# Kernel tuning notes

Hardware: AMD Instinct MI355X
Metric: run time of the kernel (lower is better)

The kernel has to match this reference:

```python
import jax, jax.numpy as jnp
import numpy as np

V, E, H, D_IMG, A = 32000, 512, 512, 2048, 128
PAD_ID = 0
LN_EPS = 1e-5


def setup_inputs() -> dict:
    key = jax.random.key(0)
    ks = jax.random.split(key, 20)
    B, S, T = 32, 49, 64
    s = 0.02
    embed = jax.random.normal(ks[0], (V, E), jnp.float32) * s
    embed = embed.at[PAD_ID].set(0.0)
    return {
        "img_seq": jax.random.normal(ks[1], (B, S, D_IMG), jnp.float32),
        "tokens_in": jax.random.randint(ks[2], (B, T), 0, V, jnp.int64),
        "embed": embed,
        "W_ctx": jax.random.normal(ks[3], (E, D_IMG), jnp.float32) * s,
        "W_mix": jax.random.normal(ks[4], (E, 2 * E), jnp.float32) * s,
        "ln_g": jnp.ones((E,), jnp.float32),
        "ln_b": jnp.zeros((E,), jnp.float32),
        "W_ih": jax.random.normal(ks[5], (4 * H, E), jnp.float32) * s,
        "W_hh": jax.random.normal(ks[6], (4 * H, H), jnp.float32) * s,
        "b_ih": jnp.zeros((4 * H,), jnp.float32),
        "b_hh": jnp.zeros((4 * H,), jnp.float32),
        "W_head": jax.random.normal(ks[7], (V, H), jnp.float32) * s,
        "W_img": jax.random.normal(ks[8], (A, D_IMG), jnp.float32) * s,
        "W_hid": jax.random.normal(ks[9], (A, H), jnp.float32) * s,
        "w_score": jax.random.normal(ks[10], (A,), jnp.float32) * s,
        "W_h0": jax.random.normal(ks[11], (H, D_IMG), jnp.float32) * s,
        "b_h0": jnp.zeros((H,), jnp.float32),
        "W_c0": jax.random.normal(ks[12], (H, D_IMG), jnp.float32) * s,
        "b_c0": jnp.zeros((H,), jnp.float32),
    }


def _decode(img_seq, tokens_in, embed, W_ctx, W_mix, ln_g, ln_b,
            W_ih, W_hh, b_ih, b_hh, W_head, W_img, W_hid, w_score,
            W_h0, b_h0, W_c0, b_c0):
    # precompute image projection: [B,S,A]
    proj_image = jnp.einsum('bsd,ad->bsa', img_seq, W_img)
    g = img_seq.mean(1)  # [B, D_img]
    h = jnp.tanh(g @ W_h0.T + b_h0) * 0.5
    c = jnp.tanh(g @ W_c0.T + b_c0) * 0.5

    def step(carry, tok_t):
        h, c = carry
        emb = embed[tok_t] * (tok_t != PAD_ID)[:, None].astype(embed.dtype)
        # additive attention
        ph = h @ W_hid.T  # [B,A]
        comb = jnp.tanh(proj_image + ph[:, None, :])  # [B,S,A]
        scores = jnp.einsum('bsa,a->bs', comb, w_score)
        w = jax.nn.softmax(scores, axis=-1)
        ctx = jnp.einsum('bs,bsd->bd', w, img_seq)
        ctxE = ctx @ W_ctx.T
        x = jnp.concatenate([emb, ctxE], axis=-1) @ W_mix.T
        x = jax.nn.relu(x)
        mu = x.mean(-1, keepdims=True)
        var = ((x - mu) ** 2).mean(-1, keepdims=True)
        x = (x - mu) * jax.lax.rsqrt(var + LN_EPS) * ln_g + ln_b
        x = x + emb
        # LSTMCell (torch gate order: i, f, g, o)
        gates = x @ W_ih.T + b_ih + h @ W_hh.T + b_hh
        i_, f_, g_, o_ = jnp.split(gates, 4, axis=-1)
        c2 = jax.nn.sigmoid(f_) * c + jax.nn.sigmoid(i_) * jnp.tanh(g_)
        h2 = jax.nn.sigmoid(o_) * jnp.tanh(c2)
        logits = h2 @ W_head.T
        return (h2, c2), logits

    _, outs = jax.lax.scan(step, (h, c), tokens_in.T)  # [T,B,V]
    return jnp.transpose(outs, (1, 0, 2))  # [B,T,V]


def reference(img_seq, tokens_in, embed, W_ctx, W_mix, ln_g, ln_b,
              W_ih, W_hh, b_ih, b_hh, W_head, W_img, W_hid, w_score,
              W_h0, b_h0, W_c0, b_c0):
    return _decode(img_seq, tokens_in, embed, W_ctx, W_mix, ln_g, ln_b,
                   W_ih, W_hh, b_ih, b_hh, W_head, W_img, W_hid, w_score,
                   W_h0, b_h0, W_c0, b_c0)
```

## Files before the change

### kernel.cpp

```cpp
#include <hip/hip_runtime.h>

#define NV 32000
#define NT 64
#define NBLK 256u

typedef unsigned long long ull;
typedef unsigned short ushort;
typedef __attribute__((ext_vector_type(8))) short v8s;
typedef __attribute__((ext_vector_type(4))) float v4f;

#define WS_WBF     0
#define WS_H2BF    8192000
#define WS_IMGEM   8716288
#define WS_PROJ    9568256
#define WS_EMBM    9781248
#define WS_WHHBF   10829824
#define WS_WIHBF   11354112
#define WS_WHIDBF  11878400
#define WS_H       11911168
#define WS_XN      11943936
#define WS_C       11960320
#define WS_FLAGS   11976704
#define WS_G       11979264
#define PS_IMGBF   0
#define PS_WCTXBF  1703936
#define PS_WIMGBF  2228224
#define PS_WMIXRBF 2359296
#define PS_WMIXLBF 2490368
#define PS_IMGEBF  3342336

__device__ __forceinline__ float fsig(float x) {
    x = fminf(fmaxf(x, -30.f), 30.f);
    return 1.f / (1.f + __expf(-x));
}
__device__ __forceinline__ float ftanh(float x) {
    x = fminf(fmaxf(x, -15.f), 15.f);
    float e = __expf(2.f * x);
    return (e - 1.f) / (e + 1.f);
}
__device__ __forceinline__ unsigned short f2bf(float f) {
    union { float f; unsigned int u; } v; v.f = f;
    unsigned int u = v.u;
    return (unsigned short)((u + 0x7FFFu + ((u >> 16) & 1u)) >> 16);
}
__device__ __forceinline__ unsigned pkf(float x, float y) {
    return (unsigned)f2bf(x) | ((unsigned)f2bf(y) << 16);
}
__device__ __forceinline__ float bf_lo(unsigned u) { return __uint_as_float(u << 16); }
__device__ __forceinline__ float bf_hi(unsigned u) { return __uint_as_float(u & 0xffff0000u); }
__device__ __forceinline__ ull agld(const ull* p) {
    return __hip_atomic_load(p, __ATOMIC_RELAXED, __HIP_MEMORY_SCOPE_AGENT);
}
__device__ __forceinline__ unsigned pk2(ull v) {
    return (unsigned)f2bf(__uint_as_float((unsigned)v)) |
           ((unsigned)f2bf(__uint_as_float((unsigned)(v >> 32))) << 16);
}


__global__ __launch_bounds__(256) void k_castall(
        const float* __restrict__ img, const float* __restrict__ Wctx,
        const float* __restrict__ Wimg, const float* __restrict__ Wmix,
        const float* __restrict__ Whh, const float* __restrict__ Wih,
        const float* __restrict__ Whid,
        ushort* __restrict__ imgbf, ushort* __restrict__ wctxbf,
        ushort* __restrict__ wimgbf, ushort* __restrict__ wmixRbf,
        ushort* __restrict__ wmixLbf, ushort* __restrict__ whhbf,
        ushort* __restrict__ wihbf, ushort* __restrict__ whidbf,
        unsigned* __restrict__ flg) {
    int blk = blockIdx.x, tid = threadIdx.x;
    if (blk >= 3616) {
        for (int i = tid; i < 2560; i += 256) flg[i] = 0u;
        return;
    }
    const float* in; ushort* out; int R, K, ldi, off;
    if (blk < 1664)      { in = img;  out = imgbf;   R = 1568; K = 2048; ldi = 2048; off = 0; }
    else if (blk < 2176) { in = Wctx; out = wctxbf;  R = 512;  K = 2048; ldi = 2048; off = 0;   blk -= 1664; }
    else if (blk < 2304) { in = Wimg; out = wimgbf;  R = 128;  K = 2048; ldi = 2048; off = 0;   blk -= 2176; }
    else if (blk < 2432) { in = Wmix; out = wmixRbf; R = 512;  K = 512;  ldi = 1024; off = 512; blk -= 2304; }
    else if (blk < 2560) { in = Wmix; out = wmixLbf; R = 512;  K = 512;  ldi = 1024; off = 0;   blk -= 2432; }
    else if (blk < 3072) { in = Whh;  out = whhbf;   R = 2048; K = 512;  ldi = 512;  off = 0;   blk -= 2560; }
    else if (blk < 3584) { in = Wih;  out = wihbf;   R = 2048; K = 512;  ldi = 512;  off = 0;   blk -= 3072; }
    else                 { in = Whid; out = whidbf;  R = 128;  K = 512;  ldi = 512;  off = 0;   blk -= 3584; }
    size_t i = ((size_t)blk * 256 + tid) * 8;
    int r = (int)(i / K), k = (int)(i % K);
    uint4 o = {0, 0, 0, 0};
    if (r < R) {
        const float* p = in + (size_t)r * ldi + off + k;
        float4 a = *(const float4*)(p);
        float4 b = *(const float4*)(p + 4);
        o.x = pkf(a.x, a.y); o.y = pkf(a.z, a.w);
        o.z = pkf(b.x, b.y); o.w = pkf(b.z, b.w);
    }
    *(uint4*)(out + i) = o;
}

__global__ __launch_bounds__(256) void k_gemm(const ushort* __restrict__ A,
        const ushort* __restrict__ B, float* __restrict__ C, int N, int K) {
    __shared__ ushort Al[128][72];
    __shared__ ushort Bl[128][72];
    int n0 = blockIdx.x * 128, m0 = blockIdx.y * 128;
    int tid = threadIdx.x, lane = tid & 63, wid = tid >> 6;
    int wm = wid >> 1, wn = wid & 1;
    v4f acc[4][4] = {};
    for (int kt = 0; kt < K; kt += 64) {
        __syncthreads();
        #pragma unroll
        for (int i = 0; i < 4; i++) {
            int idx = i * 256 + tid;
            int row = idx >> 3, c8 = (idx & 7) * 8;
            *(uint4*)&Al[row][c8] = *(const uint4*)&A[(size_t)(m0 + row) * K + kt + c8];
            *(uint4*)&Bl[row][c8] = *(const uint4*)&B[(size_t)(n0 + row) * K + kt + c8];
        }
        __syncthreads();
        #pragma unroll
        for (int kk = 0; kk < 2; kk++) {
            v8s a[4], bfr[4];
            int ko = kk * 32 + (lane >> 4) * 8;
            #pragma unroll
            for (int mi = 0; mi < 4; mi++)
                a[mi] = *(const v8s*)&Al[wm * 64 + mi * 16 + (lane & 15)][ko];
            #pragma unroll
            for (int ni = 0; ni < 4; ni++)
                bfr[ni] = *(const v8s*)&Bl[wn * 64 + ni * 16 + (lane & 15)][ko];
            #pragma unroll
            for (int mi = 0; mi < 4; mi++)
                #pragma unroll
                for (int ni = 0; ni < 4; ni++)
                    acc[mi][ni] = __builtin_amdgcn_mfma_f32_16x16x32_bf16(a[mi], bfr[ni], acc[mi][ni], 0, 0, 0);
        }
    }
    int col = lane & 15, rbase = (lane >> 4) * 4;
    #pragma unroll
    for (int mi = 0; mi < 4; mi++)
        #pragma unroll
        for (int ni = 0; ni < 4; ni++)
            #pragma unroll
            for (int r = 0; r < 4; r++) {
                int m = m0 + wm * 64 + mi * 16 + rbase + r;
                int v = n0 + wn * 64 + ni * 16 + col;
                C[(size_t)m * N + v] = acc[mi][ni][r];
            }
}

__global__ __launch_bounds__(256) void k_gemm3(
        const ushort* __restrict__ imgbf, const ushort* __restrict__ wctxbf,
        const ushort* __restrict__ wimgbf, const float* __restrict__ embed,
        const int* __restrict__ toks, const ushort* __restrict__ wmixLbf,
        ushort* __restrict__ imgEbf, float* __restrict__ proj,
        float* __restrict__ embM) {
    __shared__ ushort Al[128][72];
    __shared__ ushort Bl[128][72];
    int bid = blockIdx.x;
    const ushort* A; const ushort* B; int mode, K, N, n0, m0;
    if (bid < 52)      { mode = 0; A = imgbf; B = wctxbf;  K = 2048; N = 512; n0 = (bid & 3) * 128; m0 = (bid >> 2) * 128; }
    else if (bid < 65) { mode = 1; A = imgbf; B = wimgbf;  K = 2048; N = 128; n0 = 0;               m0 = (bid - 52) * 128; }
    else { int e = bid - 65; mode = 2; A = nullptr; B = wmixLbf; K = 512; N = 512; n0 = (e & 3) * 128; m0 = (e >> 2) * 128; }
    int tid = threadIdx.x, lane = tid & 63, wid = tid >> 6;
    int wm = wid >> 1, wn = wid & 1;
    v4f acc[4][4] = {};
    for (int kt = 0; kt < K; kt += 64) {
        __syncthreads();
        #pragma unroll
        for (int i = 0; i < 4; i++) {
            int idx = i * 256 + tid;
            int row = idx >> 3, c8 = (idx & 7) * 8;
            if (mode == 2) {
                int rowg = m0 + row;
                int tok = toks[(rowg & 31) * 64 + (rowg >> 5)];
                uint4 oa = {0, 0, 0, 0};
                if (tok != 0) {
                    const float* pa = embed + (size_t)tok * 512 + kt + c8;
                    float4 a0 = *(const float4*)pa, a1 = *(const float4*)(pa + 4);
                    oa.x = pkf(a0.x, a0.y); oa.y = pkf(a0.z, a0.w);
                    oa.z = pkf(a1.x, a1.y); oa.w = pkf(a1.z, a1.w);
                }
                *(uint4*)&Al[row][c8] = oa;
            } else {
                *(uint4*)&Al[row][c8] = *(const uint4*)&A[(size_t)(m0 + row) * K + kt + c8];
            }
            *(uint4*)&Bl[row][c8] = *(const uint4*)&B[(size_t)(n0 + row) * K + kt + c8];
        }
        __syncthreads();
        #pragma unroll
        for (int kk = 0; kk < 2; kk++) {
            v8s a[4], bfr[4];
            int ko = kk * 32 + (lane >> 4) * 8;
            #pragma unroll
            for (int mi = 0; mi < 4; mi++)
                a[mi] = *(const v8s*)&Al[wm * 64 + mi * 16 + (lane & 15)][ko];
            #pragma unroll
            for (int ni = 0; ni < 4; ni++)
                bfr[ni] = *(const v8s*)&Bl[wn * 64 + ni * 16 + (lane & 15)][ko];
            #pragma unroll
            for (int mi = 0; mi < 4; mi++)
                #pragma unroll
                for (int ni = 0; ni < 4; ni++)
                    acc[mi][ni] = __builtin_amdgcn_mfma_f32_16x16x32_bf16(a[mi], bfr[ni], acc[mi][ni], 0, 0, 0);
        }
    }
    int col = lane & 15, rbase = (lane >> 4) * 4;
    #pragma unroll
    for (int mi = 0; mi < 4; mi++)
        #pragma unroll
        for (int ni = 0; ni < 4; ni++)
            #pragma unroll
            for (int r = 0; r < 4; r++) {
                int m = m0 + wm * 64 + mi * 16 + rbase + r;
                int v = n0 + wn * 64 + ni * 16 + col;
                if (mode == 0)      imgEbf[(size_t)m * 512 + v] = f2bf(acc[mi][ni][r]);
                else if (mode == 1) proj[(size_t)m * 128 + v] = acc[mi][ni][r];
                else                embM[(size_t)m * 512 + v] = acc[mi][ni][r];
            }
}

__global__ __launch_bounds__(256) void k_gmean(const float* __restrict__ img,
                                               float* __restrict__ g) {
    int b = blockIdx.x;
    for (int d = threadIdx.x; d < 2048; d += 256) {
        float s = 0.f;
        for (int ss = 0; ss < 49; ss++) s += img[((size_t)(b * 49 + ss)) * 2048 + d];
        g[b * 2048 + d] = s * (1.f / 49.f);
    }
}

__global__ __launch_bounds__(256) void k_h0c0(const float* __restrict__ g,
        const float* __restrict__ Wh0, const float* __restrict__ bh0,
        const float* __restrict__ Wc0, const float* __restrict__ bc0,
        float* __restrict__ h0, float* __restrict__ c0) {
    int b = blockIdx.x >> 2, m = (blockIdx.x >> 1) & 1, rh = blockIdx.x & 1;
    __shared__ float gs[2048];
    for (int d = threadIdx.x; d < 2048; d += 256) gs[d] = g[b * 2048 + d];
    __syncthreads();
    const float* W = m ? Wc0 : Wh0;
    const float* bb = m ? bc0 : bh0;
    float* out = m ? c0 : h0;
    int r = rh * 256 + threadIdx.x;
    float acc = 0.f;
    const float* wr = W + (size_t)r * 2048;
    for (int d = 0; d < 2048; d += 4) {
        float4 w = *(const float4*)(wr + d);
        acc += w.x * gs[d] + w.y * gs[d + 1] + w.z * gs[d + 2] + w.w * gs[d + 3];
    }
    out[b * 512 + r] = ftanh(acc + bb[r]) * 0.5f;
}


__device__ __forceinline__ void waitflags(unsigned* FLG, int base, int stride,
                                          int n, unsigned tgt) {
    if (threadIdx.x < 64) {
        bool done;
        do {
            unsigned v = tgt;
            if ((int)threadIdx.x < n)
                v = __hip_atomic_load(FLG + (base + (int)threadIdx.x * stride) * 16,
                                      __ATOMIC_RELAXED, __HIP_MEMORY_SCOPE_AGENT);
            done = __all((int)(v >= tgt));
            if (!done) __builtin_amdgcn_s_sleep(1);
        } while (!done);
    }
    __syncthreads();
}

template <int SLP>
__device__ __forceinline__ void waitgates(unsigned* FLG, unsigned tgt) {
    if (threadIdx.x < 64) {
        bool done;
        do {
            unsigned v0 = __hip_atomic_load(FLG + threadIdx.x * 16,
                            __ATOMIC_RELAXED, __HIP_MEMORY_SCOPE_AGENT);
            unsigned v1 = __hip_atomic_load(FLG + (threadIdx.x + 64) * 16,
                            __ATOMIC_RELAXED, __HIP_MEMORY_SCOPE_AGENT);
            done = __all((int)(v0 >= tgt && v1 >= tgt));
            if (!done) __builtin_amdgcn_s_sleep(SLP);
        } while (!done);
    }
    __syncthreads();
}

__device__ __forceinline__ void waitcast(unsigned* FLG) {
    if (threadIdx.x == 0) {
        while (__hip_atomic_load(FLG + 12, __ATOMIC_RELAXED, __HIP_MEMORY_SCOPE_AGENT) < 96u)
            __builtin_amdgcn_s_sleep(4);
    }
    __syncthreads();
}

union SMem {
    struct {
        ushort wh[64][520];
        ushort wi[64][520];
        ushort hsb[16][520];
        float gtmp[4][16][16];
        ushort h2s[16][8];
    } g;
    struct {
        float imgem[49][512];
        float projl[49][128];
        float hb[512];
        float ebs[512];
        float php[8][128];
        float ph[128];
        float scp[64][16];
        float wsm[64];
        float xps[2][512];
        float wred[8][2];
        float bc[2];
    } a;
    struct {
        ushort Al[256][72];
        ushort Bl[128][72];
    } h;
};

__device__ __forceinline__ void head_tile(SMem& sm, const ushort* __restrict__ h2bf,
        const ushort* __restrict__ Wbf, float* __restrict__ out, int m0, int n0) {
    int tid = threadIdx.x, lane = tid & 63, wid = tid >> 6;
    int wm = wid >> 1, wn = wid & 1;
    v4f acc[4][4] = {};
    for (int kt = 0; kt < 512; kt += 64) {
        __syncthreads();
        #pragma unroll
        for (int i = 0; i < 2; i++) {
            int idx = i * 1024 + tid;
            int row = idx >> 3, c8 = (idx & 7) * 8;
            const ull* p = (const ull*)&h2bf[(size_t)(m0 + row) * 512 + kt + c8];
            ull v0 = agld(p), v1 = agld(p + 1);
            *(ull*)&sm.h.Al[row][c8] = v0;
            *(ull*)&sm.h.Al[row][c8 + 4] = v1;
        }
        {
            int row = tid >> 3, c8 = (tid & 7) * 8;
            *(uint4*)&sm.h.Bl[row][c8] = *(const uint4*)&Wbf[(size_t)(n0 + row) * 512 + kt + c8];
        }
        __syncthreads();
        if (wid < 8) {
            #pragma unroll
            for (int kk = 0; kk < 2; kk++) {
                v8s a[4], bfr[4];
                int ko = kk * 32 + (lane >> 4) * 8;
                #pragma unroll
                for (int mi = 0; mi < 4; mi++)
                    a[mi] = *(const v8s*)&sm.h.Al[wm * 64 + mi * 16 + (lane & 15)][ko];
                #pragma unroll
                for (int ni = 0; ni < 4; ni++)
                    bfr[ni] = *(const v8s*)&sm.h.Bl[wn * 64 + ni * 16 + (lane & 15)][ko];
                #pragma unroll
                for (int mi = 0; mi < 4; mi++)
                    #pragma unroll
                    for (int ni = 0; ni < 4; ni++)
                        acc[mi][ni] = __builtin_amdgcn_mfma_f32_16x16x32_bf16(a[mi], bfr[ni], acc[mi][ni], 0, 0, 0);
            }
        }
    }
    if (wid < 8) {
        int col = lane & 15, rbase = (lane >> 4) * 4;
        #pragma unroll
        for (int mi = 0; mi < 4; mi++)
            #pragma unroll
            for (int ni = 0; ni < 4; ni++)
                #pragma unroll
                for (int r = 0; r < 4; r++) {
                    int m = m0 + wm * 64 + mi * 16 + rbase + r;
                    int v = n0 + wn * 64 + ni * 16 + col;
                    int b = m & 31, t = m >> 5;
                    out[((size_t)(b * 64 + t)) * 32000 + v] = acc[mi][ni][r];
                }
    }
}

__global__ __launch_bounds__(1024, 1) void k_persist(
        const int* __restrict__ toks, const float* __restrict__ embed,
        const float* __restrict__ lng, const float* __restrict__ lnb,
        const float* __restrict__ bih, const float* __restrict__ bhh,
        const float* __restrict__ wsc, const ushort* __restrict__ whidbf,
        const ushort* __restrict__ whhbf, const ushort* __restrict__ wihbf,
        const float* __restrict__ proj, const float* __restrict__ imgEM,
        const float* __restrict__ embM, float* __restrict__ H,
        const float* __restrict__ C0, float* __restrict__ XN,
        unsigned* __restrict__ FLG, ushort* __restrict__ h2bf,
        const float* __restrict__ W_head, ushort* __restrict__ Wbf,
        float* __restrict__ out) {
    __shared__ SMem sm;
    __shared__ unsigned sh_w;
    int blk = blockIdx.x, tid = threadIdx.x;

    if (blk < 128) {
        int jc = blk >> 2, bg = blk & 3, b0 = bg * 8;
        int wid = tid >> 6, lane = tid & 63;
        int gate = wid & 3;
        for (int i = tid; i < 4096; i += 1024) {
            int rr = i >> 6, c8 = (i & 63) * 8;
            size_t R = (size_t)((rr >> 4) * 512 + jc * 16 + (rr & 15)) * 512 + c8;
            *(uint4*)&sm.g.wh[rr][c8] = *(const uint4*)&whhbf[R];
            *(uint4*)&sm.g.wi[rr][c8] = *(const uint4*)&wihbf[R];
        }
        for (int i = tid; i < 2080; i += 1024) ((ull*)sm.g.hsb)[i] = 0;
        float c_reg = 0.f, bs0 = 0.f, bs1 = 0.f, bs2 = 0.f, bs3 = 0.f;
        if (tid < 128) {
            int jl = tid >> 3, bb = tid & 7;
            int j = jc * 16 + jl;
            c_reg = C0[(b0 + bb) * 512 + j];
            bs0 = bih[j] + bhh[j];
            bs1 = bih[512 + j] + bhh[512 + j];
            bs2 = bih[1024 + j] + bhh[1024 + j];
            bs3 = bih[1536 + j] + bhh[1536 + j];
        }
        __syncthreads();

        for (int t = 0; t < NT; t++) {
            waitflags(FLG, bg, 4, 32, (unsigned)t);
            {
                const float* Hb = H + (t & 1) * 16384 + b0 * 512;
                if (tid < 512) {
                    int bb = tid >> 6, c8 = (tid & 63) * 8;
                    const ull* p = (const ull*)(Hb + bb * 512 + c8);
                    uint4 o = { pk2(agld(p)), pk2(agld(p + 1)),
                                pk2(agld(p + 2)), pk2(agld(p + 3)) };
                    *(uint4*)&sm.g.hsb[bb][c8] = o;
                }
            }
            __syncthreads();
            v4f acc = {};
            if (wid < 4) {
                #pragma unroll
                for (int ks = 0; ks < 16; ks++) {
                    int ko = ks * 32 + (lane >> 4) * 8;
                    v8s a = *(const v8s*)&sm.g.hsb[lane & 15][ko];
                    v8s b = *(const v8s*)&sm.g.wh[gate * 16 + (lane & 15)][ko];
                    acc = __builtin_amdgcn_mfma_f32_16x16x32_bf16(a, b, acc, 0, 0, 0);
                }
            }
            waitflags(FLG, 128 + b0, 1, 8, (unsigned)(t + 1));
            {
                const float* Xb = XN + b0 * 512;
                if (tid < 512) {
                    int bb = tid >> 6, c8 = (tid & 63) * 8;
                    const ull* p = (const ull*)(Xb + bb * 512 + c8);
                    uint4 o = { pk2(agld(p)), pk2(agld(p + 1)),
                                pk2(agld(p + 2)), pk2(agld(p + 3)) };
                    *(uint4*)&sm.g.hsb[bb][c8] = o;
                }
            }
            __syncthreads();
            if (wid < 4) {
                #pragma unroll
                for (int ks = 0; ks < 16; ks++) {
                    int ko = ks * 32 + (lane >> 4) * 8;
                    v8s a = *(const v8s*)&sm.g.hsb[lane & 15][ko];
                    v8s b = *(const v8s*)&sm.g.wi[gate * 16 + (lane & 15)][ko];
                    acc = __builtin_amdgcn_mfma_f32_16x16x32_bf16(a, b, acc, 0, 0, 0);
                }
                #pragma unroll
                for (int q = 0; q < 4; q++)
                    sm.g.gtmp[gate][lane & 15][(lane >> 4) * 4 + q] = acc[q];
            }
            __syncthreads();
            if (tid < 128) {
                int jl = tid >> 3, bb = tid & 7;
                float vi = sm.g.gtmp[0][jl][bb] + bs0;
                float vf = sm.g.gtmp[1][jl][bb] + bs1;
                float vg = sm.g.gtmp[2][jl][bb] + bs2;
                float vo = sm.g.gtmp[3][jl][bb] + bs3;
                float c2 = fsig(vf) * c_reg + fsig(vi) * ftanh(vg);
                float h2 = fsig(vo) * ftanh(c2);
                c_reg = c2;
                int bglob = b0 + bb, j = jc * 16 + jl;
                __hip_atomic_store((unsigned*)&H[((t + 1) & 1) * 16384 + bglob * 512 + j],
                                   __float_as_uint(h2), __ATOMIC_RELAXED, __HIP_MEMORY_SCOPE_AGENT);
                sm.g.h2s[jl][bb] = f2bf(h2);
            }
            __syncthreads();
            if (tid < 64) {
                int jlp = tid >> 3, bb = tid & 7;
                unsigned pk = (unsigned)sm.g.h2s[2 * jlp][bb]
                            | ((unsigned)sm.g.h2s[2 * jlp + 1][bb] << 16);
                int bglob = b0 + bb, j = jc * 16 + 2 * jlp;
                __hip_atomic_store((unsigned*)&h2bf[(size_t)(t * 32 + bglob) * 512 + j],
                                   pk, __ATOMIC_RELAXED, __HIP_MEMORY_SCOPE_AGENT);
            }
            __syncthreads();
            if (tid == 0)
                __hip_atomic_store(FLG + blk * 16, (unsigned)(t + 1),
                                   __ATOMIC_RELAXED, __HIP_MEMORY_SCOPE_AGENT);
        }
    } else if (blk < 160) {
        int b = blk - 128, bgb = b >> 3;
        for (int i = tid; i < 49 * 512; i += 1024)
            sm.a.imgem[i >> 9][i & 511] = imgEM[(size_t)b * 49 * 512 + i];
        for (int i = tid; i < 49 * 128; i += 1024)
            sm.a.projl[i >> 7][i & 127] = proj[(size_t)b * 49 * 128 + i];
        __syncthreads();
        for (int t = 0; t < NT; t++) {
            waitflags(FLG, bgb, 4, 32, (unsigned)t);
            int tok = toks[b * 64 + t];
            if (tid < 256) {
                ull v = agld((const ull*)(H + (t & 1) * 16384) + b * 256 + tid);
                *(ull*)&sm.a.hb[tid * 2] = v;
            } else if (tid < 768) {
                int k = tid - 256;
                sm.a.ebs[k] = (tok == 0) ? 0.f : embed[(size_t)tok * 512 + k];
            }
            __syncthreads();
            {
                int a = tid & 127, kq = tid >> 7;
                const ushort* wr2 = whidbf + (size_t)a * 512 + kq * 64;
                const float* hp = sm.a.hb + kq * 64;
                float p = 0.f;
                #pragma unroll
                for (int k = 0; k < 64; k += 8) {
                    uint4 q = *(const uint4*)(wr2 + k);
                    float4 ha = *(const float4*)(hp + k);
                    float4 hb4 = *(const float4*)(hp + k + 4);
                    p += bf_lo(q.x)*ha.x + bf_hi(q.x)*ha.y + bf_lo(q.y)*ha.z + bf_hi(q.y)*ha.w
                       + bf_lo(q.z)*hb4.x + bf_hi(q.z)*hb4.y + bf_lo(q.w)*hb4.z + bf_hi(q.w)*hb4.w;
                }
                sm.a.php[kq][a] = p;
            }
            __syncthreads();
            if (tid < 128) {
                float p = 0.f;
                #pragma unroll
                for (int kq = 0; kq < 8; kq++) p += sm.a.php[kq][tid];
                sm.a.ph[tid] = p;
            }
            __syncthreads();
            {
                int s = tid >> 4, aq = tid & 15;
                float p = 0.f;
                if (s < 49) {
                    const float* pr = &sm.a.projl[s][aq * 8];
                    #pragma unroll
                    for (int a = 0; a < 8; a++)
                        p += ftanh(pr[a] + sm.a.ph[aq * 8 + a]) * wsc[aq * 8 + a];
                }
                sm.a.scp[s][aq] = p;
            }
            __syncthreads();
            if (tid < 64) {
                float v = 0.f;
                #pragma unroll
                for (int q = 0; q < 16; q++) v += sm.a.scp[tid][q];
                if (tid >= 49) v = -1e30f;
                float m = v;
                for (int o = 32; o > 0; o >>= 1) m = fmaxf(m, __shfl_xor(m, o));
                float e = (tid < 49) ? __expf(v - m) : 0.f;
                float su = e;
                for (int o = 32; o > 0; o >>= 1) su += __shfl_xor(su, o);
                sm.a.wsm[tid] = e / su;
            }
            __syncthreads();
            {
                int e = tid & 511, sh = tid >> 9;
                float xp = 0.f;
                if (sh == 0) xp = embM[(size_t)(t * 32 + b) * 512 + e];
                int s0 = sh * 25, s1 = sh ? 49 : 25;
                for (int s = s0; s < s1; s++)
                    xp += sm.a.wsm[s] * sm.a.imgem[s][e];
                sm.a.xps[sh][e] = xp;
            }
            __syncthreads();
            if (tid < 512) {
                float x = fmaxf(sm.a.xps[0][tid] + sm.a.xps[1][tid], 0.f);
                float s = x, s2 = x * x;
                for (int o = 32; o > 0; o >>= 1) { s += __shfl_xor(s, o); s2 += __shfl_xor(s2, o); }
                if ((tid & 63) == 0) { sm.a.wred[tid >> 6][0] = s; sm.a.wred[tid >> 6][1] = s2; }
            }
            __syncthreads();
            if (tid == 0) {
                float s = 0.f, s2 = 0.f;
                #pragma unroll
                for (int w = 0; w < 8; w++) { s += sm.a.wred[w][0]; s2 += sm.a.wred[w][1]; }
                float mu = s * (1.f / 512.f);
                float var = s2 * (1.f / 512.f) - mu * mu;
                sm.a.bc[0] = mu; sm.a.bc[1] = rsqrtf(var + 1e-5f);
            }
            __syncthreads();
            if (tid < 512) {
                float x = fmaxf(sm.a.xps[0][tid] + sm.a.xps[1][tid], 0.f);
                float xn = (x - sm.a.bc[0]) * sm.a.bc[1] * lng[tid] + lnb[tid] + sm.a.ebs[tid];
                __hip_atomic_store((unsigned*)&XN[b * 512 + tid], __float_as_uint(xn),
                                   __ATOMIC_RELAXED, __HIP_MEMORY_SCOPE_AGENT);
            }
            __syncthreads();
            if (tid == 0)
                __hip_atomic_store(FLG + (128 + b) * 16, (unsigned)(t + 1),
                                   __ATOMIC_RELAXED, __HIP_MEMORY_SCOPE_AGENT);
        }
    } else {
        int hb = blk - 160;
        {
            ull* wq = (ull*)Wbf;
            for (size_t i = (size_t)hb * 1024 + tid; i < 4096000; i += 98304) {
                const float* p = W_head + i * 4;
                float4 a = *(const float4*)p;
                ull v = (ull)pkf(a.x, a.y) | ((ull)pkf(a.z, a.w) << 32);
                __hip_atomic_store(wq + i, v, __ATOMIC_RELAXED, __HIP_MEMORY_SCOPE_AGENT);
            }
            __syncthreads();
            if (tid == 0)
                __hip_atomic_fetch_add(FLG + 12, 1u, __ATOMIC_RELAXED,
                                       __HIP_MEMORY_SCOPE_AGENT);
        }
        waitcast(FLG);
        unsigned have = 0;
        for (int w = hb; w < 1750; w += 96) {
            int mt = w / 250, nt = w % 250;
            unsigned need = (unsigned)(mt * 8 + 8);
            if (have < need) { waitgates<8>(FLG, need); have = need; }
            head_tile(sm, h2bf, (const ushort*)Wbf, out, mt * 256, nt * 128);
        }
    }

    waitgates<2>(FLG, (unsigned)NT);
    waitcast(FLG);
    for (;;) {
        if (tid == 0)
            sh_w = __hip_atomic_fetch_add(FLG + 8, 1u, __ATOMIC_RELAXED,
                                          __HIP_MEMORY_SCOPE_AGENT);
        __syncthreads();
        unsigned w = sh_w;
        __syncthreads();
        if (w >= 250u) break;
        head_tile(sm, h2bf, (const ushort*)Wbf, out, 7 * 256, (int)w * 128);
    }
}

extern "C" void kernel_launch(void* const* d_in, const int* in_sizes, int n_in,
                              void* d_out, int out_size, void* d_ws, size_t ws_size,
                              hipStream_t stream) {
    const float* img    = (const float*)d_in[0];
    const int*   toks   = (const int*)d_in[1];
    const float* embed  = (const float*)d_in[2];
    const float* W_ctx  = (const float*)d_in[3];
    const float* W_mix  = (const float*)d_in[4];
    const float* ln_g   = (const float*)d_in[5];
    const float* ln_b   = (const float*)d_in[6];
    const float* W_ih   = (const float*)d_in[7];
    const float* W_hh   = (const float*)d_in[8];
    const float* b_ih   = (const float*)d_in[9];
    const float* b_hh   = (const float*)d_in[10];
    const float* W_head = (const float*)d_in[11];
    const float* W_img  = (const float*)d_in[12];
    const float* W_hid  = (const float*)d_in[13];
    const float* w_sc   = (const float*)d_in[14];
    const float* W_h0   = (const float*)d_in[15];
    const float* b_h0   = (const float*)d_in[16];
    const float* W_c0   = (const float*)d_in[17];
    const float* b_c0   = (const float*)d_in[18];

    float* out = (float*)d_out;
    float* ws  = (float*)d_ws;
    ushort* Wbf    = (ushort*)(ws + WS_WBF);
    ushort* h2bf   = (ushort*)(ws + WS_H2BF);
    float*  imgEM  = ws + WS_IMGEM;
    float*  proj   = ws + WS_PROJ;
    float*  embM   = ws + WS_EMBM;
    ushort* whhbf  = (ushort*)(ws + WS_WHHBF);
    ushort* wihbf  = (ushort*)(ws + WS_WIHBF);
    ushort* whidbf = (ushort*)(ws + WS_WHIDBF);
    float*  H      = ws + WS_H;
    float*  XN     = ws + WS_XN;
    float*  C      = ws + WS_C;
    unsigned* flg  = (unsigned*)(ws + WS_FLAGS);
    float*  g      = ws + WS_G;
    ushort* imgbf   = (ushort*)(ws + PS_IMGBF);
    ushort* wctxbf  = (ushort*)(ws + PS_WCTXBF);
    ushort* wimgbf  = (ushort*)(ws + PS_WIMGBF);
    ushort* wmixRbf = (ushort*)(ws + PS_WMIXRBF);
    ushort* wmixLbf = (ushort*)(ws + PS_WMIXLBF);
    ushort* imgEbf  = (ushort*)(ws + PS_IMGEBF);

    k_castall<<<3617, 256, 0, stream>>>(img, W_ctx, W_img, W_mix, W_hh, W_ih, W_hid,
                                        imgbf, wctxbf, wimgbf, wmixRbf, wmixLbf,
                                        whhbf, wihbf, whidbf, flg);
    k_gemm3<<<129, 256, 0, stream>>>(imgbf, wctxbf, wimgbf, embed, toks, wmixLbf,
                                     imgEbf, proj, embM);
    k_gemm<<<dim3(4, 13), 256, 0, stream>>>(imgEbf, wmixRbf, imgEM, 512, 512);
    k_gmean<<<32, 256, 0, stream>>>(img, g);
    k_h0c0<<<128, 256, 0, stream>>>(g, W_h0, b_h0, W_c0, b_c0, H, C);

    k_persist<<<NBLK, 1024, 0, stream>>>(toks, embed, ln_g, ln_b, b_ih, b_hh, w_sc,
                                         whidbf, whhbf, wihbf, proj, imgEM, embM,
                                         H, C, XN, flg, h2bf, W_head, Wbf, out);
}
```

Before: 906.7 us.

## Fold h0/c0 init into batched MFMA gemm and store LN output as bf16

Removes the separate scalar fp32 h0/c0 kernel. W_h0 and W_c0 are now cast to bf16 in the cast kernel, and the h0/c0 projections run as extra MFMA tile blocks inside k_gemm3, with tanh applied in the epilogue. Separately, the layer-normed x vector exchanged between blocks each step is now written as packed bf16 instead of fp32, which halves the cross-block traffic on the recurrent critical path. The costs are extra cast work, padded 128-row tiles for only 32 real rows, and bf16 rounding of h0/c0.

```diff
diff --git a/kernel.cpp b/kernel.cpp
--- a/kernel.cpp
+++ b/kernel.cpp
@@ -28,6 +28,8 @@
 #define PS_WMIXRBF 2359296
 #define PS_WMIXLBF 2490368
 #define PS_IMGEBF  3342336
+#define PS_WH0BF   3768320
+#define PS_WC0BF   4292608
 
 __device__ __forceinline__ float fsig(float x) {
     x = fminf(fmaxf(x, -30.f), 30.f);
@@ -61,14 +63,16 @@
         const float* __restrict__ img, const float* __restrict__ Wctx,
         const float* __restrict__ Wimg, const float* __restrict__ Wmix,
         const float* __restrict__ Whh, const float* __restrict__ Wih,
-        const float* __restrict__ Whid,
+        const float* __restrict__ Whid, const float* __restrict__ Wh0,
+        const float* __restrict__ Wc0,
         ushort* __restrict__ imgbf, ushort* __restrict__ wctxbf,
         ushort* __restrict__ wimgbf, ushort* __restrict__ wmixRbf,
         ushort* __restrict__ wmixLbf, ushort* __restrict__ whhbf,
         ushort* __restrict__ wihbf, ushort* __restrict__ whidbf,
+        ushort* __restrict__ wh0bf, ushort* __restrict__ wc0bf,
         unsigned* __restrict__ flg) {
     int blk = blockIdx.x, tid = threadIdx.x;
-    if (blk >= 3616) {
+    if (blk >= 4640) {
         for (int i = tid; i < 2560; i += 256) flg[i] = 0u;
         return;
     }
@@ -80,7 +84,9 @@
     else if (blk < 2560) { in = Wmix; out = wmixLbf; R = 512;  K = 512;  ldi = 1024; off = 0;   blk -= 2432; }
     else if (blk < 3072) { in = Whh;  out = whhbf;   R = 2048; K = 512;  ldi = 512;  off = 0;   blk -= 2560; }
     else if (blk < 3584) { in = Wih;  out = wihbf;   R = 2048; K = 512;  ldi = 512;  off = 0;   blk -= 3072; }
-    else                 { in = Whid; out = whidbf;  R = 128;  K = 512;  ldi = 512;  off = 0;   blk -= 3584; }
+    else if (blk < 3616) { in = Whid; out = whidbf;  R = 128;  K = 512;  ldi = 512;  off = 0;   blk -= 3584; }
+    else if (blk < 4128) { in = Wh0;  out = wh0bf;   R = 512;  K = 2048; ldi = 2048; off = 0;   blk -= 3616; }
+    else                 { in = Wc0;  out = wc0bf;   R = 512;  K = 2048; ldi = 2048; off = 0;   blk -= 4128; }
     size_t i = ((size_t)blk * 256 + tid) * 8;
     int r = (int)(i / K), k = (int)(i % K);
     uint4 o = {0, 0, 0, 0};
@@ -146,15 +152,21 @@
         const ushort* __restrict__ imgbf, const ushort* __restrict__ wctxbf,
         const ushort* __restrict__ wimgbf, const float* __restrict__ embed,
         const int* __restrict__ toks, const ushort* __restrict__ wmixLbf,
+        const ushort* __restrict__ wh0bf, const ushort* __restrict__ wc0bf,
+        const float* __restrict__ g, const float* __restrict__ bh0,
+        const float* __restrict__ bc0,
         ushort* __restrict__ imgEbf, float* __restrict__ proj,
-        float* __restrict__ embM) {
+        float* __restrict__ embM, float* __restrict__ Hout,
+        float* __restrict__ Cout) {
     __shared__ ushort Al[128][72];
     __shared__ ushort Bl[128][72];
     int bid = blockIdx.x;
     const ushort* A; const ushort* B; int mode, K, N, n0, m0;
-    if (bid < 52)      { mode = 0; A = imgbf; B = wctxbf;  K = 2048; N = 512; n0 = (bid & 3) * 128; m0 = (bid >> 2) * 128; }
-    else if (bid < 65) { mode = 1; A = imgbf; B = wimgbf;  K = 2048; N = 128; n0 = 0;               m0 = (bid - 52) * 128; }
-    else { int e = bid - 65; mode = 2; A = nullptr; B = wmixLbf; K = 512; N = 512; n0 = (e & 3) * 128; m0 = (e >> 2) * 128; }
+    if (bid < 52)       { mode = 0; A = imgbf; B = wctxbf;  K = 2048; N = 512; n0 = (bid & 3) * 128; m0 = (bid >> 2) * 128; }
+    else if (bid < 65)  { mode = 1; A = imgbf; B = wimgbf;  K = 2048; N = 128; n0 = 0;               m0 = (bid - 52) * 128; }
+    else if (bid < 129) { int e = bid - 65;  mode = 2; A = nullptr; B = wmixLbf; K = 512;  N = 512; n0 = (e & 3) * 128; m0 = (e >> 2) * 128; }
+    else if (bid < 133) { mode = 3; A = nullptr; B = wh0bf; K = 2048; N = 512; n0 = (bid - 129) * 128; m0 = 0; }
+    else                { mode = 4; A = nullptr; B = wc0bf; K = 2048; N = 512; n0 = (bid - 133) * 128; m0 = 0; }
     int tid = threadIdx.x, lane = tid & 63, wid = tid >> 6;
     int wm = wid >> 1, wn = wid & 1;
     v4f acc[4][4] = {};
@@ -175,6 +187,16 @@
                     oa.z = pkf(a1.x, a1.y); oa.w = pkf(a1.z, a1.w);
                 }
                 *(uint4*)&Al[row][c8] = oa;
+            } else if (mode >= 3) {
+                int rowg = m0 + row;
+                uint4 oa = {0, 0, 0, 0};
+                if (rowg < 32) {
+                    const float* pa = g + (size_t)rowg * 2048 + kt + c8;
+                    float4 a0 = *(const float4*)pa, a1 = *(const float4*)(pa + 4);
+                    oa.x = pkf(a0.x, a0.y); oa.y = pkf(a0.z, a0.w);
+                    oa.z = pkf(a1.x, a1.y); oa.w = pkf(a1.z, a1.w);
+                }
+                *(uint4*)&Al[row][c8] = oa;
             } else {
                 *(uint4*)&Al[row][c8] = *(const uint4*)&A[(size_t)(m0 + row) * K + kt + c8];
             }
@@ -209,7 +231,13 @@
                 int v = n0 + wn * 64 + ni * 16 + col;
                 if (mode == 0)      imgEbf[(size_t)m * 512 + v] = f2bf(acc[mi][ni][r]);
                 else if (mode == 1) proj[(size_t)m * 128 + v] = acc[mi][ni][r];
-                else                embM[(size_t)m * 512 + v] = acc[mi][ni][r];
+                else if (mode == 2) embM[(size_t)m * 512 + v] = acc[mi][ni][r];
+                else if (m < 32) {
+                    float pre = acc[mi][ni][r] + ((mode == 3) ? bh0[v] : bc0[v]);
+                    float val = ftanh(pre) * 0.5f;
+                    if (mode == 3) Hout[m * 512 + v] = val;
+                    else           Cout[m * 512 + v] = val;
+                }
             }
 }
 
@@ -221,27 +249,6 @@
         for (int ss = 0; ss < 49; ss++) s += img[((size_t)(b * 49 + ss)) * 2048 + d];
         g[b * 2048 + d] = s * (1.f / 49.f);
     }
-}
-
-__global__ __launch_bounds__(256) void k_h0c0(const float* __restrict__ g,
-        const float* __restrict__ Wh0, const float* __restrict__ bh0,
-        const float* __restrict__ Wc0, const float* __restrict__ bc0,
-        float* __restrict__ h0, float* __restrict__ c0) {
-    int b = blockIdx.x >> 2, m = (blockIdx.x >> 1) & 1, rh = blockIdx.x & 1;
-    __shared__ float gs[2048];
-    for (int d = threadIdx.x; d < 2048; d += 256) gs[d] = g[b * 2048 + d];
-    __syncthreads();
-    const float* W = m ? Wc0 : Wh0;
-    const float* bb = m ? bc0 : bh0;
-    float* out = m ? c0 : h0;
-    int r = rh * 256 + threadIdx.x;
-    float acc = 0.f;
-    const float* wr = W + (size_t)r * 2048;
-    for (int d = 0; d < 2048; d += 4) {
-        float4 w = *(const float4*)(wr + d);
-        acc += w.x * gs[d] + w.y * gs[d + 1] + w.z * gs[d + 2] + w.w * gs[d + 3];
-    }
-    out[b * 512 + r] = ftanh(acc + bb[r]) * 0.5f;
 }
 
 
@@ -376,7 +383,7 @@
         const ushort* __restrict__ whhbf, const ushort* __restrict__ wihbf,
         const float* __restrict__ proj, const float* __restrict__ imgEM,
         const float* __restrict__ embM, float* __restrict__ H,
-        const float* __restrict__ C0, float* __restrict__ XN,
+        const float* __restrict__ C0, ushort* __restrict__ XNh,
         unsigned* __restrict__ FLG, ushort* __restrict__ h2bf,
         const float* __restrict__ W_head, ushort* __restrict__ Wbf,
         float* __restrict__ out) {
@@ -432,13 +439,13 @@
             }
             waitflags(FLG, 128 + b0, 1, 8, (unsigned)(t + 1));
             {
-                const float* Xb = XN + b0 * 512;
+                const ushort* Xh = XNh + b0 * 512;
                 if (tid < 512) {
                     int bb = tid >> 6, c8 = (tid & 63) * 8;
-                    const ull* p = (const ull*)(Xb + bb * 512 + c8);
-                    uint4 o = { pk2(agld(p)), pk2(agld(p + 1)),
-                                pk2(agld(p + 2)), pk2(agld(p + 3)) };
-                    *(uint4*)&sm.g.hsb[bb][c8] = o;
+                    const ull* p = (const ull*)(Xh + bb * 512 + c8);
+                    ull v0 = agld(p), v1 = agld(p + 1);
+                    *(ull*)&sm.g.hsb[bb][c8] = v0;
+                    *(ull*)&sm.g.hsb[bb][c8 + 4] = v1;
                 }
             }
             __syncthreads();
@@ -578,8 +585,12 @@
             if (tid < 512) {
                 float x = fmaxf(sm.a.xps[0][tid] + sm.a.xps[1][tid], 0.f);
                 float xn = (x - sm.a.bc[0]) * sm.a.bc[1] * lng[tid] + lnb[tid] + sm.a.ebs[tid];
-                __hip_atomic_store((unsigned*)&XN[b * 512 + tid], __float_as_uint(xn),
-                                   __ATOMIC_RELAXED, __HIP_MEMORY_SCOPE_AGENT);
+                float xnn = __shfl_xor(xn, 1);
+                if (!(tid & 1)) {
+                    unsigned pkv = pkf(xn, xnn);
+                    __hip_atomic_store((unsigned*)&XNh[b * 512 + tid], pkv,
+                                       __ATOMIC_RELAXED, __HIP_MEMORY_SCOPE_AGENT);
+                }
             }
             __syncthreads();
             if (tid == 0)
@@ -659,7 +670,7 @@
     ushort* wihbf  = (ushort*)(ws + WS_WIHBF);
     ushort* whidbf = (ushort*)(ws + WS_WHIDBF);
     float*  H      = ws + WS_H;
-    float*  XN     = ws + WS_XN;
+    ushort* XNh    = (ushort*)(ws + WS_XN);
     float*  C      = ws + WS_C;
     unsigned* flg  = (unsigned*)(ws + WS_FLAGS);
     float*  g      = ws + WS_G;
@@ -669,17 +680,20 @@
     ushort* wmixRbf = (ushort*)(ws + PS_WMIXRBF);
     ushort* wmixLbf = (ushort*)(ws + PS_WMIXLBF);
     ushort* imgEbf  = (ushort*)(ws + PS_IMGEBF);
-
-    k_castall<<<3617, 256, 0, stream>>>(img, W_ctx, W_img, W_mix, W_hh, W_ih, W_hid,
+    ushort* wh0bf   = (ushort*)(ws + PS_WH0BF);
+    ushort* wc0bf   = (ushort*)(ws + PS_WC0BF);
+
+    k_castall<<<4641, 256, 0, stream>>>(img, W_ctx, W_img, W_mix, W_hh, W_ih, W_hid,
+                                        W_h0, W_c0,
                                         imgbf, wctxbf, wimgbf, wmixRbf, wmixLbf,
-                                        whhbf, wihbf, whidbf, flg);
-    k_gemm3<<<129, 256, 0, stream>>>(imgbf, wctxbf, wimgbf, embed, toks, wmixLbf,
-                                     imgEbf, proj, embM);
+                                        whhbf, wihbf, whidbf, wh0bf, wc0bf, flg);
+    k_gmean<<<32, 256, 0, stream>>>(img, g);
+    k_gemm3<<<137, 256, 0, stream>>>(imgbf, wctxbf, wimgbf, embed, toks, wmixLbf,
+                                     wh0bf, wc0bf, g, b_h0, b_c0,
+                                     imgEbf, proj, embM, H, C);
     k_gemm<<<dim3(4, 13), 256, 0, stream>>>(imgEbf, wmixRbf, imgEM, 512, 512);
-    k_gmean<<<32, 256, 0, stream>>>(img, g);
-    k_h0c0<<<128, 256, 0, stream>>>(g, W_h0, b_h0, W_c0, b_c0, H, C);
 
     k_persist<<<NBLK, 1024, 0, stream>>>(toks, embed, ln_g, ln_b, b_ih, b_hh, w_sc,
                                          whidbf, whhbf, wihbf, proj, imgEM, embM,
-                                         H, C, XN, flg, h2bf, W_head, Wbf, out);
-}
+                                         H, C, XNh, flg, h2bf, W_head, Wbf, out);
+}
```

After: 834.8 us. -7.9%, faster.
